# Kernel optimization log

Hardware: AMD Instinct MI355X
Metric: run time of the kernel (lower is better)

## Reference

```python
import jax, jax.numpy as jnp
import numpy as np

N = 200000   # nodes
E = 600000   # edges
D = 128      # input_channels
H = 128      # hidden_channels
EPS = 1e-5   # BatchNorm1d eps


def setup_inputs() -> dict:
    key = jax.random.key(0)
    ks = jax.random.split(key, 6)
    x = jax.random.normal(ks[0], (N, D), dtype=jnp.float32)
    edge_index = jax.random.randint(ks[1], (2, E), 0, N)
    a1 = jnp.full((1,), 0.25, dtype=jnp.float32)   # PReLU init
    gamma = jnp.ones((D,), dtype=jnp.float32)
    beta = jnp.zeros((D,), dtype=jnp.float32)
    W1 = jax.random.normal(ks[2], (D, H), dtype=jnp.float32) / np.float32(np.sqrt(D))
    b1 = jnp.zeros((H,), dtype=jnp.float32)
    a2 = jnp.full((1,), 0.25, dtype=jnp.float32)
    W2 = jax.random.normal(ks[3], (H, D), dtype=jnp.float32) / np.float32(np.sqrt(H))
    b2 = jnp.zeros((D,), dtype=jnp.float32)
    return dict(x=x, edge_index=edge_index, a1=a1, gamma=gamma, beta=beta,
                W1=W1, b1=b1, a2=a2, W2=W2, b2=b2)


def _prelu(x, a):
    return jnp.where(x >= 0, x, a[0] * x)


def _batchnorm(x, gamma, beta):
    # training-mode BatchNorm1d: batch mean, biased variance
    mean = jnp.mean(x, axis=0)
    var = jnp.mean(jnp.square(x - mean), axis=0)
    return (x - mean) * jax.lax.rsqrt(var + EPS) * gamma + beta


def _gcn_conv(x, W, b, src, dst, n):
    # PyG GCNConv: add self-loops, symmetric normalization D^-1/2 (A+I) D^-1/2
    h = x @ W                                            # [n, out]
    deg = jnp.ones((n,), h.dtype).at[dst].add(1.0)       # degree incl. self-loop
    dinv = jax.lax.rsqrt(deg)
    coef = (dinv[src] * dinv[dst])[:, None]              # [E, 1]
    msg = h[src] * coef                                  # gather  [E, out]
    out = jax.ops.segment_sum(msg, dst, num_segments=n)  # scatter [n, out]
    out = out + h * (1.0 / deg)[:, None]                 # self-loop term
    return out + b


def reference(x, edge_index, a1, gamma, beta, W1, b1, a2, W2, b2):
    src, dst = edge_index[0], edge_index[1]
    n = x.shape[0]
    h = _prelu(x, a1)
    h = _batchnorm(h, gamma, beta)
    h = _gcn_conv(h, W1, b1, src, dst, n)
    h = _prelu(h, a2)
    h = _gcn_conv(h, W2, b2, src, dst, n)
    return h
```

## Files before the change

kernel.cpp:

```cpp
#include <hip/hip_runtime.h>

#define NN 200000
#define NE 600000
#define DD 128
#define GT 1563

constexpr float BN_EPS = 1e-5f;

typedef unsigned short u16;
typedef short bf16x8 __attribute__((ext_vector_type(8)));
typedef float f32x4  __attribute__((ext_vector_type(4)));
typedef float f32x2  __attribute__((ext_vector_type(2)));


__global__ void k_zero(int* __restrict__ cnt, float* __restrict__ ssum, float* __restrict__ ssq) {
  int i = blockIdx.x*256 + threadIdx.x;
  if (i < NN) cnt[i] = 0;
  if (i < DD) { ssum[i] = 0.f; ssq[i] = 0.f; }
}

__global__ void k_count(const int* __restrict__ ei, int* __restrict__ cnt) {
  int e = blockIdx.x*256 + threadIdx.x;
  if (e < NE) atomicAdd(&cnt[ei[NE + e]], 1);
}

__global__ void k_stats(const float* __restrict__ x, const float* __restrict__ a1p,
                        float* __restrict__ ssum, float* __restrict__ ssq) {
  __shared__ float s1[8][128], s2[8][128];
  const int c4 = (threadIdx.x & 31) * 4;
  const int rg = threadIdx.x >> 5;
  float a1 = *a1p;
  float acc1[4] = {0.f,0.f,0.f,0.f}, acc2[4] = {0.f,0.f,0.f,0.f};
  const int stride = gridDim.x * 8;
  for (int r = blockIdx.x*8 + rg; r < NN; r += stride) {
    float4 v = *(const float4*)(x + (size_t)r*DD + c4);
    float vv[4] = {v.x, v.y, v.z, v.w};
    #pragma unroll
    for (int i = 0; i < 4; ++i) {
      float u = vv[i];
      u = (u >= 0.f) ? u : a1*u;
      acc1[i] += u; acc2[i] += u*u;
    }
  }
  *(float4*)&s1[rg][c4] = make_float4(acc1[0], acc1[1], acc1[2], acc1[3]);
  *(float4*)&s2[rg][c4] = make_float4(acc2[0], acc2[1], acc2[2], acc2[3]);
  __syncthreads();
  if (threadIdx.x < 128) {
    int col = threadIdx.x;
    float t1 = 0.f, t2 = 0.f;
    #pragma unroll
    for (int g = 0; g < 8; ++g) { t1 += s1[g][col]; t2 += s2[g][col]; }
    atomicAdd(&ssum[col], t1);
    atomicAdd(&ssq [col], t2);
  }
}

__global__ void k_bn_tw1(const float* __restrict__ ssum, const float* __restrict__ ssq,
                         const float* __restrict__ gamma, const float* __restrict__ beta,
                         const float* __restrict__ W1,
                         float* __restrict__ sarr, float* __restrict__ tarr,
                         float* __restrict__ tw1) {
  __shared__ float ts[128];
  int j = threadIdx.x;
  float mean = ssum[j] * (1.f/NN);
  float var  = ssq[j] * (1.f/NN) - mean*mean;
  float s = gamma[j] * rsqrtf(var + BN_EPS);
  float t = beta[j] - mean*s;
  sarr[j] = s; tarr[j] = t; ts[j] = t;
  __syncthreads();
  float acc = 0.f;
  #pragma unroll 8
  for (int k = 0; k < 128; ++k) acc += ts[k] * W1[k*DD + j];
  tw1[j] = acc;
}

__global__ void k_wprep(const float* __restrict__ W, const float* __restrict__ s,
                        u16* __restrict__ hi, u16* __restrict__ lo) {
  int idx = blockIdx.x*256 + threadIdx.x;
  int j = idx >> 7, k = idx & 127;
  float v = W[(size_t)k*DD + j];
  if (s) v *= s[k];
  unsigned hb = __float_as_uint(v) & 0xffff0000u;
  float r = v - __uint_as_float(hb);
  hi[idx] = (u16)(hb >> 16);
  lo[idx] = (u16)(__float_as_uint(r) >> 16);
}


__global__ void k_scan1(const int* __restrict__ cnt, int* __restrict__ rp, int* __restrict__ bsums) {
  __shared__ int sm[256];
  int tid = threadIdx.x;
  int base = blockIdx.x*1024 + tid*4;
  int4 v = make_int4(0,0,0,0);
  if (base + 3 < NN) v = *(const int4*)(cnt + base);
  else {
    if (base   < NN) v.x = cnt[base];
    if (base+1 < NN) v.y = cnt[base+1];
    if (base+2 < NN) v.z = cnt[base+2];
    if (base+3 < NN) v.w = cnt[base+3];
  }
  int p1 = v.x, p2 = p1 + v.y, p3 = p2 + v.z, tsum = p3 + v.w;
  sm[tid] = tsum; __syncthreads();
  for (int off = 1; off < 256; off <<= 1) {
    int t = (tid >= off) ? sm[tid - off] : 0; __syncthreads();
    sm[tid] += t; __syncthreads();
  }
  int inc = sm[tid];
  int excl = inc - tsum;
  if (base   < NN) rp[base]   = excl;
  if (base+1 < NN) rp[base+1] = excl + p1;
  if (base+2 < NN) rp[base+2] = excl + p2;
  if (base+3 < NN) rp[base+3] = excl + p3;
  if (tid == 255) bsums[blockIdx.x] = inc;
}

__global__ void k_scan2(int* __restrict__ bsums, int nb) {
  __shared__ int sm[256];
  int tid = threadIdx.x;
  int v = (tid < nb) ? bsums[tid] : 0;
  sm[tid] = v; __syncthreads();
  for (int off = 1; off < 256; off <<= 1) {
    int t = (tid >= off) ? sm[tid - off] : 0; __syncthreads();
    sm[tid] += t; __syncthreads();
  }
  if (tid < nb) bsums[tid] = sm[tid] - v;
}

__global__ void k_scan3(int* __restrict__ rp, const int* __restrict__ bsums,
                        int* __restrict__ cur, const int* __restrict__ cnt,
                        float* __restrict__ dinv) {
  int i = blockIdx.x*256 + threadIdx.x;
  if (i < NN) {
    int val = rp[i] + bsums[i >> 10];
    rp[i] = val; cur[i] = val;
    dinv[i] = rsqrtf((float)(cnt[i] + 1));
  }
  if (i == 0) rp[NN] = NE;
}

__global__ void k_fill(const int* __restrict__ ei, const float* __restrict__ dinv,
                       int* __restrict__ cur, int2* __restrict__ pairs) {
  int e = blockIdx.x*256 + threadIdx.x;
  if (e < NE) {
    int s = ei[e], d = ei[NE + e];
    int pos = atomicAdd(&cur[d], 1);
    float cf = dinv[s] * dinv[d];
    pairs[pos] = make_int2(s, __float_as_int(cf));
  }
}


template<bool FUSE, bool ADDROW>
__global__ __launch_bounds__(256)
void k_gemm(const float* __restrict__ A,
            const u16* __restrict__ wt_hi, const u16* __restrict__ wt_lo,
            float* __restrict__ C,
            const float* __restrict__ tw1, const float* __restrict__ a1p)
{
  __shared__ u16 Bh[128][136];
  __shared__ u16 Bl[128][136];
  const int tid = threadIdx.x;

  #pragma unroll
  for (int i = 0; i < 8; ++i) {
    int c = tid + i*256;
    int row = c >> 4, slot = c & 15;
    *(uint4*)&Bh[row][slot*8] = ((const uint4*)wt_hi)[c];
    *(uint4*)&Bl[row][slot*8] = ((const uint4*)wt_lo)[c];
  }

  float a1v = 0.f;
  if constexpr (FUSE) a1v = *a1p;

  const int lane = tid & 63;
  const int wv   = tid >> 6;
  const int lr   = lane & 15;
  const int lk   = lane >> 4;
  const int r0   = blockIdx.x*128 + wv*32;

  f32x4 acc[2][8];
  #pragma unroll
  for (int s = 0; s < 2; ++s)
    #pragma unroll
    for (int j = 0; j < 8; ++j) acc[s][j] = (f32x4){0.f,0.f,0.f,0.f};

  __syncthreads();

  #pragma unroll
  for (int kc = 0; kc < 4; ++kc) {
    bf16x8 ah[2], al[2];
    #pragma unroll
    for (int s = 0; s < 2; ++s) {
      int r = r0 + s*16 + lr; r = (r < NN) ? r : (NN-1);
      const float* ap = A + (size_t)r*DD + kc*32 + lk*8;
      float4 v0 = *(const float4*)ap;
      float4 v1 = *(const float4*)(ap + 4);
      float vv[8] = {v0.x,v0.y,v0.z,v0.w,v1.x,v1.y,v1.z,v1.w};
      #pragma unroll
      for (int e = 0; e < 8; ++e) {
        float v = vv[e];
        if constexpr (FUSE) v = (v >= 0.f) ? v : a1v*v;
        unsigned hb = __float_as_uint(v) & 0xffff0000u;
        float rres = v - __uint_as_float(hb);
        ah[s][e] = (short)(hb >> 16);
        al[s][e] = (short)(__float_as_uint(rres) >> 16);
      }
    }
    #pragma unroll
    for (int j = 0; j < 8; ++j) {
      int wrow = j*16 + lr;
      bf16x8 bh = *(const bf16x8*)&Bh[wrow][kc*32 + lk*8];
      bf16x8 bl = *(const bf16x8*)&Bl[wrow][kc*32 + lk*8];
      #pragma unroll
      for (int s = 0; s < 2; ++s) {
        acc[s][j] = __builtin_amdgcn_mfma_f32_16x16x32_bf16(ah[s], bh, acc[s][j], 0, 0, 0);
        acc[s][j] = __builtin_amdgcn_mfma_f32_16x16x32_bf16(ah[s], bl, acc[s][j], 0, 0, 0);
        acc[s][j] = __builtin_amdgcn_mfma_f32_16x16x32_bf16(al[s], bh, acc[s][j], 0, 0, 0);
      }
    }
  }

  float tw[8];
  #pragma unroll
  for (int j = 0; j < 8; ++j) tw[j] = 0.f;
  if constexpr (ADDROW) {
    #pragma unroll
    for (int j = 0; j < 8; ++j) tw[j] = tw1[j*16 + lr];
  }

  #pragma unroll
  for (int s = 0; s < 2; ++s) {
    #pragma unroll
    for (int g = 0; g < 4; ++g) {
      int row = r0 + s*16 + lk*4 + g;
      if (row < NN) {
        float* cp = C + (size_t)row*DD + lr;
        #pragma unroll
        for (int j = 0; j < 8; ++j) cp[j*16] = acc[s][j][g] + tw[j];
      }
    }
  }
}


__global__ __launch_bounds__(256)
void k_fagg(const float* __restrict__ h, const int* __restrict__ rp,
            const int2* __restrict__ pairs,
            const u16* __restrict__ w2h, const u16* __restrict__ w2l,
            const float* __restrict__ b1, const float* __restrict__ a2p,
            float* __restrict__ h2)
{
  __shared__ u16 Ghi[32][136];
  __shared__ u16 Glo[32][136];
  const int wave = threadIdx.x >> 6;
  const int lane = threadIdx.x & 63;
  const int nbB  = blockIdx.x * 32;
  const int nb   = nbB + wave*8;
  const float2* hv = (const float2*)h;

  int rv = 0;
  if (lane < 9) rv = rp[nb + lane];
  int beg[8], cnt8[8];
  #pragma unroll
  for (int i = 0; i < 8; ++i) {
    int b0 = __builtin_amdgcn_readfirstlane(__shfl(rv, i));
    int b1v = __builtin_amdgcn_readfirstlane(__shfl(rv, i+1));
    beg[i] = b0; cnt8[i] = b1v - b0;
  }

  float2 b = ((const float2*)b1)[lane];
  float2 acc[8];
  #pragma unroll
  for (int i = 0; i < 8; ++i) {
    float2 self = hv[(size_t)(nb+i)*64 + lane];
    float sc = 1.f / (float)(cnt8[i] + 1);
    acc[i].x = sc*self.x + b.x;
    acc[i].y = sc*self.y + b.y;
  }

  int maxc = 0;
  #pragma unroll
  for (int i = 0; i < 8; ++i) maxc = max(maxc, cnt8[i]);

  for (int c = 0; c < maxc; ++c) {
    int2 p[8];
    #pragma unroll
    for (int i = 0; i < 8; ++i)
      if (c < cnt8[i]) p[i] = pairs[beg[i] + c];
    #pragma unroll
    for (int i = 0; i < 8; ++i)
      if (c < cnt8[i]) {
        float2 g = hv[(size_t)p[i].x*64 + lane];
        float cf = __int_as_float(p[i].y);
        acc[i].x += cf*g.x; acc[i].y += cf*g.y;
      }
  }

  float a2 = *a2p;
  #pragma unroll
  for (int i = 0; i < 8; ++i) {
    float ax = acc[i].x, ay = acc[i].y;
    ax = (ax >= 0.f) ? ax : a2*ax;
    ay = (ay >= 0.f) ? ay : a2*ay;
    unsigned hx = __float_as_uint(ax) & 0xffff0000u;
    unsigned hy = __float_as_uint(ay) & 0xffff0000u;
    float rx = ax - __uint_as_float(hx);
    float ry = ay - __uint_as_float(hy);
    unsigned hiw = (hx >> 16) | hy;
    unsigned low = (__float_as_uint(rx) >> 16) | (__float_as_uint(ry) & 0xffff0000u);
    int row = wave*8 + i;
    *(unsigned*)&Ghi[row][lane*2] = hiw;
    *(unsigned*)&Glo[row][lane*2] = low;
  }
  __syncthreads();

  const int lr = lane & 15, lk = lane >> 4;
  f32x4 dacc[2][2];
  #pragma unroll
  for (int s = 0; s < 2; ++s)
    #pragma unroll
    for (int t = 0; t < 2; ++t) dacc[s][t] = (f32x4){0.f,0.f,0.f,0.f};

  #pragma unroll
  for (int kc = 0; kc < 4; ++kc) {
    bf16x8 ah0 = *(const bf16x8*)&Ghi[lr]   [kc*32 + lk*8];
    bf16x8 al0 = *(const bf16x8*)&Glo[lr]   [kc*32 + lk*8];
    bf16x8 ah1 = *(const bf16x8*)&Ghi[16+lr][kc*32 + lk*8];
    bf16x8 al1 = *(const bf16x8*)&Glo[16+lr][kc*32 + lk*8];
    #pragma unroll
    for (int t = 0; t < 2; ++t) {
      int wrow = wave*32 + t*16 + lr;
      bf16x8 bh = *(const bf16x8*)(w2h + (size_t)wrow*DD + kc*32 + lk*8);
      bf16x8 bl = *(const bf16x8*)(w2l + (size_t)wrow*DD + kc*32 + lk*8);
      dacc[0][t] = __builtin_amdgcn_mfma_f32_16x16x32_bf16(ah0, bh, dacc[0][t], 0, 0, 0);
      dacc[0][t] = __builtin_amdgcn_mfma_f32_16x16x32_bf16(ah0, bl, dacc[0][t], 0, 0, 0);
      dacc[0][t] = __builtin_amdgcn_mfma_f32_16x16x32_bf16(al0, bh, dacc[0][t], 0, 0, 0);
      dacc[1][t] = __builtin_amdgcn_mfma_f32_16x16x32_bf16(ah1, bh, dacc[1][t], 0, 0, 0);
      dacc[1][t] = __builtin_amdgcn_mfma_f32_16x16x32_bf16(ah1, bl, dacc[1][t], 0, 0, 0);
      dacc[1][t] = __builtin_amdgcn_mfma_f32_16x16x32_bf16(al1, bh, dacc[1][t], 0, 0, 0);
    }
  }

  #pragma unroll
  for (int s = 0; s < 2; ++s)
    #pragma unroll
    for (int t = 0; t < 2; ++t)
      #pragma unroll
      for (int g = 0; g < 4; ++g) {
        int row = nbB + s*16 + lk*4 + g;
        h2[(size_t)row*DD + wave*32 + t*16 + lr] = dacc[s][t][g];
      }
}


template<bool PRELU>
__global__ __launch_bounds__(256)
void k_agg(const float* __restrict__ h, const int* __restrict__ rp,
           const int2* __restrict__ pairs,
           const float* __restrict__ bias, const float* __restrict__ a2p,
           float* __restrict__ out)
{
  const int wave = threadIdx.x >> 6;
  const int lane = threadIdx.x & 63;
  const int nb = (blockIdx.x*4 + wave) * 8;
  if (nb >= NN) return;
  const float2* h2 = (const float2*)h;
  f32x2* o2 = (f32x2*)out;

  int rv = 0;
  if (lane < 9) rv = rp[nb + lane];
  int beg[8], cnt8[8];
  #pragma unroll
  for (int i = 0; i < 8; ++i) {
    int b0 = __builtin_amdgcn_readfirstlane(__shfl(rv, i));
    int b1 = __builtin_amdgcn_readfirstlane(__shfl(rv, i+1));
    beg[i] = b0; cnt8[i] = b1 - b0;
  }

  float2 b = ((const float2*)bias)[lane];
  float a2 = 1.f;
  if constexpr (PRELU) a2 = *a2p;

  float2 acc[8];
  #pragma unroll
  for (int i = 0; i < 8; ++i) {
    float2 self = h2[(size_t)(nb+i)*64 + lane];
    float sc = 1.f / (float)(cnt8[i] + 1);
    acc[i].x = sc*self.x + b.x;
    acc[i].y = sc*self.y + b.y;
  }

  int maxc = 0;
  #pragma unroll
  for (int i = 0; i < 8; ++i) maxc = max(maxc, cnt8[i]);

  for (int c = 0; c < maxc; ++c) {
    int2 p[8];
    #pragma unroll
    for (int i = 0; i < 8; ++i)
      if (c < cnt8[i]) p[i] = pairs[beg[i] + c];
    #pragma unroll
    for (int i = 0; i < 8; ++i)
      if (c < cnt8[i]) {
        float2 g = h2[(size_t)p[i].x*64 + lane];
        float cf = __int_as_float(p[i].y);
        acc[i].x += cf*g.x; acc[i].y += cf*g.y;
      }
  }

  #pragma unroll
  for (int i = 0; i < 8; ++i) {
    float ax = acc[i].x, ay = acc[i].y;
    if constexpr (PRELU) {
      ax = (ax >= 0.f) ? ax : a2*ax;
      ay = (ay >= 0.f) ? ay : a2*ay;
    }
    f32x2 o; o[0] = ax; o[1] = ay;
    __builtin_nontemporal_store(o, &o2[(size_t)(nb+i)*64 + lane]);
  }
}


extern "C" void kernel_launch(void* const* d_in, const int* in_sizes, int n_in,
                              void* d_out, int out_size, void* d_ws, size_t ws_size,
                              hipStream_t stream) {
  const float* x     = (const float*)d_in[0];
  const int*   ei    = (const int*)  d_in[1];
  const float* a1    = (const float*)d_in[2];
  const float* gamma = (const float*)d_in[3];
  const float* beta  = (const float*)d_in[4];
  const float* W1    = (const float*)d_in[5];
  const float* b1    = (const float*)d_in[6];
  const float* a2    = (const float*)d_in[7];
  const float* W2    = (const float*)d_in[8];
  const float* b2    = (const float*)d_in[9];
  float* out = (float*)d_out;

  char* w = (char*)d_ws;
  auto alloc = [&](size_t bytes) { char* p = w; w += (bytes + 255) & ~(size_t)255; return p; };
  float* hbuf  = (float*)alloc((size_t)NN*DD*4);
  float* dinv  = (float*)alloc((size_t)NN*4);
  int*   cnt   = (int*)  alloc((size_t)NN*4);
  int*   rp    = (int*)  alloc((size_t)(NN+1)*4);
  int*   cur   = (int*)  alloc((size_t)NN*4);
  int2*  pairs = (int2*) alloc((size_t)NE*8);
  int*   bsums = (int*)  alloc(256*4);
  float* ssum  = (float*)alloc(128*4);
  float* ssq   = (float*)alloc(128*4);
  float* sarr  = (float*)alloc(128*4);
  float* tarr  = (float*)alloc(128*4);
  float* tw1   = (float*)alloc(128*4);
  u16*   w1h   = (u16*)  alloc(128*128*2);
  u16*   w1l   = (u16*)  alloc(128*128*2);
  u16*   w2h   = (u16*)  alloc(128*128*2);
  u16*   w2l   = (u16*)  alloc(128*128*2);
  float* hbuf2 = (float*)alloc((size_t)NN*DD*4);
  const bool fused = ((size_t)(w - (char*)d_ws) <= ws_size);

  const int nblkN = (NN + 255)/256;
  const int nblkE = (NE + 255)/256;
  const int nblkA = NN/32;
  const int nblkF = NN/32;

  k_zero  <<<nblkN, 256, 0, stream>>>(cnt, ssum, ssq);
  k_count <<<nblkE, 256, 0, stream>>>(ei, cnt);
  k_stats <<<1024,  256, 0, stream>>>(x, a1, ssum, ssq);
  k_bn_tw1<<<1,     128, 0, stream>>>(ssum, ssq, gamma, beta, W1, sarr, tarr, tw1);
  k_wprep <<<64,    256, 0, stream>>>(W2, nullptr, w2h, w2l);
  k_wprep <<<64,    256, 0, stream>>>(W1, sarr,    w1h, w1l);
  k_scan1 <<<196,   256, 0, stream>>>(cnt, rp, bsums);
  k_scan2 <<<1,     256, 0, stream>>>(bsums, 196);
  k_scan3 <<<nblkN, 256, 0, stream>>>(rp, bsums, cur, cnt, dinv);
  k_fill  <<<nblkE, 256, 0, stream>>>(ei, dinv, cur, pairs);

  k_gemm<true, true><<<GT, 256, 0, stream>>>(x, w1h, w1l, hbuf, tw1, a1);
  if (fused) {
    k_fagg<<<nblkF, 256, 0, stream>>>(hbuf, rp, pairs, w2h, w2l, b1, a2, hbuf2);
    k_agg<false><<<nblkA, 256, 0, stream>>>(hbuf2, rp, pairs, b2, nullptr, out);
  } else {
    k_agg<true >         <<<nblkA, 256, 0, stream>>>(hbuf, rp, pairs, b1, a2, out);
    k_gemm<false, false><<<GT, 256, 0, stream>>>(out, w2h, w2l, hbuf, nullptr, nullptr);
    k_agg<false>         <<<nblkA, 256, 0, stream>>>(hbuf, rp, pairs, b2, nullptr, out);
  }
}
```

Baseline: 503.5 us.

## Record edge slot in count pass, factor dinv[dst] out, per-wave fused GEMM

```diff
diff --git a/kernel.cpp b/kernel.cpp
--- a/kernel.cpp
+++ b/kernel.cpp
@@ -19,9 +19,9 @@
   if (i < DD) { ssum[i] = 0.f; ssq[i] = 0.f; }
 }
 
-__global__ void k_count(const int* __restrict__ ei, int* __restrict__ cnt) {
+__global__ void k_count(const int* __restrict__ ei, int* __restrict__ cnt, int* __restrict__ pos) {
   int e = blockIdx.x*256 + threadIdx.x;
-  if (e < NE) atomicAdd(&cnt[ei[NE + e]], 1);
+  if (e < NE) pos[e] = atomicAdd(&cnt[ei[NE + e]], 1);
 }
 
 __global__ void k_stats(const float* __restrict__ x, const float* __restrict__ a1p,
@@ -127,25 +127,23 @@
 }
 
 __global__ void k_scan3(int* __restrict__ rp, const int* __restrict__ bsums,
-                        int* __restrict__ cur, const int* __restrict__ cnt,
-                        float* __restrict__ dinv) {
+                        const int* __restrict__ cnt, float* __restrict__ dinv) {
   int i = blockIdx.x*256 + threadIdx.x;
   if (i < NN) {
-    int val = rp[i] + bsums[i >> 10];
-    rp[i] = val; cur[i] = val;
+    rp[i] += bsums[i >> 10];
     dinv[i] = rsqrtf((float)(cnt[i] + 1));
   }
   if (i == 0) rp[NN] = NE;
 }
 
 __global__ void k_fill(const int* __restrict__ ei, const float* __restrict__ dinv,
-                       int* __restrict__ cur, int2* __restrict__ pairs) {
+                       const int* __restrict__ rp, const int* __restrict__ pos,
+                       int2* __restrict__ pairs) {
   int e = blockIdx.x*256 + threadIdx.x;
   if (e < NE) {
     int s = ei[e], d = ei[NE + e];
-    int pos = atomicAdd(&cur[d], 1);
-    float cf = dinv[s] * dinv[d];
-    pairs[pos] = make_int2(s, __float_as_int(cf));
+    int slot = rp[d] + pos[e];
+    pairs[slot] = make_int2(s, __float_as_int(dinv[s]));
   }
 }
 
@@ -250,12 +248,11 @@
             const float* __restrict__ b1, const float* __restrict__ a2p,
             float* __restrict__ h2)
 {
-  __shared__ u16 Ghi[32][136];
-  __shared__ u16 Glo[32][136];
+  __shared__ u16 Ghi[4][8][152];
+  __shared__ u16 Glo[4][8][152];
   const int wave = threadIdx.x >> 6;
   const int lane = threadIdx.x & 63;
-  const int nbB  = blockIdx.x * 32;
-  const int nb   = nbB + wave*8;
+  const int nb   = (blockIdx.x*4 + wave) * 8;
   const float2* hv = (const float2*)h;
 
   int rv = 0;
@@ -268,15 +265,9 @@
     beg[i] = b0; cnt8[i] = b1v - b0;
   }
 
-  float2 b = ((const float2*)b1)[lane];
   float2 acc[8];
   #pragma unroll
-  for (int i = 0; i < 8; ++i) {
-    float2 self = hv[(size_t)(nb+i)*64 + lane];
-    float sc = 1.f / (float)(cnt8[i] + 1);
-    acc[i].x = sc*self.x + b.x;
-    acc[i].y = sc*self.y + b.y;
-  }
+  for (int i = 0; i < 8; ++i) acc[i] = make_float2(0.f, 0.f);
 
   int maxc = 0;
   #pragma unroll
@@ -297,9 +288,15 @@
   }
 
   float a2 = *a2p;
+  float2 b = ((const float2*)b1)[lane];
   #pragma unroll
   for (int i = 0; i < 8; ++i) {
-    float ax = acc[i].x, ay = acc[i].y;
+    float2 self = hv[(size_t)(nb+i)*64 + lane];
+    float deg = (float)(cnt8[i] + 1);
+    float dd = rsqrtf(deg);
+    float sc = 1.f / deg;
+    float ax = dd*acc[i].x + sc*self.x + b.x;
+    float ay = dd*acc[i].y + sc*self.y + b.y;
     ax = (ax >= 0.f) ? ax : a2*ax;
     ay = (ay >= 0.f) ? ay : a2*ay;
     unsigned hx = __float_as_uint(ax) & 0xffff0000u;
@@ -308,48 +305,40 @@
     float ry = ay - __uint_as_float(hy);
     unsigned hiw = (hx >> 16) | hy;
     unsigned low = (__float_as_uint(rx) >> 16) | (__float_as_uint(ry) & 0xffff0000u);
-    int row = wave*8 + i;
-    *(unsigned*)&Ghi[row][lane*2] = hiw;
-    *(unsigned*)&Glo[row][lane*2] = low;
-  }
-  __syncthreads();
+    *(unsigned*)&Ghi[wave][i][lane*2] = hiw;
+    *(unsigned*)&Glo[wave][i][lane*2] = low;
+  }
 
   const int lr = lane & 15, lk = lane >> 4;
-  f32x4 dacc[2][2];
-  #pragma unroll
-  for (int s = 0; s < 2; ++s)
-    #pragma unroll
-    for (int t = 0; t < 2; ++t) dacc[s][t] = (f32x4){0.f,0.f,0.f,0.f};
+  const int ar = lr & 7;
+  f32x4 dacc[8];
+  #pragma unroll
+  for (int t = 0; t < 8; ++t) dacc[t] = (f32x4){0.f,0.f,0.f,0.f};
 
   #pragma unroll
   for (int kc = 0; kc < 4; ++kc) {
-    bf16x8 ah0 = *(const bf16x8*)&Ghi[lr]   [kc*32 + lk*8];
-    bf16x8 al0 = *(const bf16x8*)&Glo[lr]   [kc*32 + lk*8];
-    bf16x8 ah1 = *(const bf16x8*)&Ghi[16+lr][kc*32 + lk*8];
-    bf16x8 al1 = *(const bf16x8*)&Glo[16+lr][kc*32 + lk*8];
-    #pragma unroll
-    for (int t = 0; t < 2; ++t) {
-      int wrow = wave*32 + t*16 + lr;
+    bf16x8 ah = *(const bf16x8*)&Ghi[wave][ar][kc*32 + lk*8];
+    bf16x8 al = *(const bf16x8*)&Glo[wave][ar][kc*32 + lk*8];
+    #pragma unroll
+    for (int t = 0; t < 8; ++t) {
+      int wrow = t*16 + lr;
       bf16x8 bh = *(const bf16x8*)(w2h + (size_t)wrow*DD + kc*32 + lk*8);
       bf16x8 bl = *(const bf16x8*)(w2l + (size_t)wrow*DD + kc*32 + lk*8);
-      dacc[0][t] = __builtin_amdgcn_mfma_f32_16x16x32_bf16(ah0, bh, dacc[0][t], 0, 0, 0);
-      dacc[0][t] = __builtin_amdgcn_mfma_f32_16x16x32_bf16(ah0, bl, dacc[0][t], 0, 0, 0);
-      dacc[0][t] = __builtin_amdgcn_mfma_f32_16x16x32_bf16(al0, bh, dacc[0][t], 0, 0, 0);
-      dacc[1][t] = __builtin_amdgcn_mfma_f32_16x16x32_bf16(ah1, bh, dacc[1][t], 0, 0, 0);
-      dacc[1][t] = __builtin_amdgcn_mfma_f32_16x16x32_bf16(ah1, bl, dacc[1][t], 0, 0, 0);
-      dacc[1][t] = __builtin_amdgcn_mfma_f32_16x16x32_bf16(al1, bh, dacc[1][t], 0, 0, 0);
-    }
-  }
-
-  #pragma unroll
-  for (int s = 0; s < 2; ++s)
-    #pragma unroll
-    for (int t = 0; t < 2; ++t)
+      dacc[t] = __builtin_amdgcn_mfma_f32_16x16x32_bf16(ah, bh, dacc[t], 0, 0, 0);
+      dacc[t] = __builtin_amdgcn_mfma_f32_16x16x32_bf16(ah, bl, dacc[t], 0, 0, 0);
+      dacc[t] = __builtin_amdgcn_mfma_f32_16x16x32_bf16(al, bh, dacc[t], 0, 0, 0);
+    }
+  }
+
+  if (lk < 2) {
+    #pragma unroll
+    for (int g = 0; g < 4; ++g) {
+      int row = nb + lk*4 + g;
+      float* cp = h2 + (size_t)row*DD + lr;
       #pragma unroll
-      for (int g = 0; g < 4; ++g) {
-        int row = nbB + s*16 + lk*4 + g;
-        h2[(size_t)row*DD + wave*32 + t*16 + lr] = dacc[s][t][g];
-      }
+      for (int t = 0; t < 8; ++t) cp[t*16] = dacc[t][g];
+    }
+  }
 }
 
 
@@ -383,12 +372,7 @@
 
   float2 acc[8];
   #pragma unroll
-  for (int i = 0; i < 8; ++i) {
-    float2 self = h2[(size_t)(nb+i)*64 + lane];
-    float sc = 1.f / (float)(cnt8[i] + 1);
-    acc[i].x = sc*self.x + b.x;
-    acc[i].y = sc*self.y + b.y;
-  }
+  for (int i = 0; i < 8; ++i) acc[i] = make_float2(0.f, 0.f);
 
   int maxc = 0;
   #pragma unroll
@@ -410,7 +394,12 @@
 
   #pragma unroll
   for (int i = 0; i < 8; ++i) {
-    float ax = acc[i].x, ay = acc[i].y;
+    float2 self = h2[(size_t)(nb+i)*64 + lane];
+    float deg = (float)(cnt8[i] + 1);
+    float dd = rsqrtf(deg);
+    float sc = 1.f / deg;
+    float ax = dd*acc[i].x + sc*self.x + b.x;
+    float ay = dd*acc[i].y + sc*self.y + b.y;
     if constexpr (PRELU) {
       ax = (ax >= 0.f) ? ax : a2*ax;
       ay = (ay >= 0.f) ? ay : a2*ay;
@@ -442,7 +431,7 @@
   float* dinv  = (float*)alloc((size_t)NN*4);
   int*   cnt   = (int*)  alloc((size_t)NN*4);
   int*   rp    = (int*)  alloc((size_t)(NN+1)*4);
-  int*   cur   = (int*)  alloc((size_t)NN*4);
+  int*   pos   = (int*)  alloc((size_t)NE*4);
   int2*  pairs = (int2*) alloc((size_t)NE*8);
   int*   bsums = (int*)  alloc(256*4);
   float* ssum  = (float*)alloc(128*4);
@@ -460,22 +449,21 @@
   const int nblkN = (NN + 255)/256;
   const int nblkE = (NE + 255)/256;
   const int nblkA = NN/32;
-  const int nblkF = NN/32;
 
   k_zero  <<<nblkN, 256, 0, stream>>>(cnt, ssum, ssq);
-  k_count <<<nblkE, 256, 0, stream>>>(ei, cnt);
+  k_count <<<nblkE, 256, 0, stream>>>(ei, cnt, pos);
   k_stats <<<1024,  256, 0, stream>>>(x, a1, ssum, ssq);
   k_bn_tw1<<<1,     128, 0, stream>>>(ssum, ssq, gamma, beta, W1, sarr, tarr, tw1);
   k_wprep <<<64,    256, 0, stream>>>(W2, nullptr, w2h, w2l);
   k_wprep <<<64,    256, 0, stream>>>(W1, sarr,    w1h, w1l);
   k_scan1 <<<196,   256, 0, stream>>>(cnt, rp, bsums);
   k_scan2 <<<1,     256, 0, stream>>>(bsums, 196);
-  k_scan3 <<<nblkN, 256, 0, stream>>>(rp, bsums, cur, cnt, dinv);
-  k_fill  <<<nblkE, 256, 0, stream>>>(ei, dinv, cur, pairs);
+  k_scan3 <<<nblkN, 256, 0, stream>>>(rp, bsums, cnt, dinv);
+  k_fill  <<<nblkE, 256, 0, stream>>>(ei, dinv, rp, pos, pairs);
 
   k_gemm<true, true><<<GT, 256, 0, stream>>>(x, w1h, w1l, hbuf, tw1, a1);
   if (fused) {
-    k_fagg<<<nblkF, 256, 0, stream>>>(hbuf, rp, pairs, w2h, w2l, b1, a2, hbuf2);
+    k_fagg<<<nblkA, 256, 0, stream>>>(hbuf, rp, pairs, w2h, w2l, b1, a2, hbuf2);
     k_agg<false><<<nblkA, 256, 0, stream>>>(hbuf2, rp, pairs, b2, nullptr, out);
   } else {
     k_agg<true >         <<<nblkA, 256, 0, stream>>>(hbuf, rp, pairs, b1, a2, out);
```

Result: slower. 609.3 us (+21.0%).
